# Kernel tuning notes

Measured on AMD Instinct MI355X. Metric: run time of the kernel, lower is better.

Reference implementation:

```python
import jax, jax.numpy as jnp
import numpy as np

ALPHA = 0.2  # LeakyReLU negative slope

def setup_inputs() -> dict:
    key = jax.random.key(0)
    k1, k2, k3, k4 = jax.random.split(key, 4)
    B, N, IN_C, OUT_C = 4, 4096, 64, 64
    features = jax.random.normal(k1, (B, N, IN_C), dtype=jnp.float32)
    adj = jax.random.uniform(k2, (B, N, N), dtype=jnp.float32)  # unused by the module's math
    # xavier_normal approximations
    W = jax.random.normal(k3, (IN_C, OUT_C), dtype=jnp.float32) * np.sqrt(2.0 / (IN_C + OUT_C))
    a = jax.random.normal(k4, (2 * OUT_C, 1), dtype=jnp.float32) * np.sqrt(2.0 / (2 * OUT_C + 1))
    return {"features": features, "adj": adj, "W": W, "a": a}

def reference(features, adj, W, a):
    # h: [B, N, F]
    h = jnp.matmul(features, W)
    out_c = W.shape[1]
    a1 = a[:out_c, 0]   # [F]
    a2 = a[out_c:, 0]   # [F]
    # e[b,i,j] = leakyrelu(h_i . a1 + h_j . a2)  (decomposed; avoids O(N^2*2F) concat)
    s1 = jnp.einsum('bnf,f->bn', h, a1)  # [B, N]
    s2 = jnp.einsum('bnf,f->bn', h, a2)  # [B, N]
    e = s1[:, :, None] + s2[:, None, :]  # [B, N, N]
    e = jnp.where(e >= 0, e, ALPHA * e)  # leaky relu
    attention = jax.nn.softmax(e, axis=2)  # note: adj is NOT used (faithful to source)
    h_prime = jnp.matmul(attention, h)  # [B, N, F]
    return h_prime
```

## Files before the change

kernel.cpp:

```cpp
#include <hip/hip_runtime.h>
#include <hip/hip_bf16.h>
#include <cmath>

#define LRALPHA 0.2f

namespace {
constexpr int BB = 4;
constexpr int NN = 4096;
constexpr int ROWS = BB * NN;
}

typedef __attribute__((ext_vector_type(8))) short bf16x8;
typedef __attribute__((ext_vector_type(4))) float f32x4;

static __device__ inline short f2bf(float x) {
  __hip_bfloat16 t = __float2bfloat16(x);
  return *reinterpret_cast<short*>(&t);
}
static __device__ inline float bf2f(short x) {
  __hip_bfloat16 t = *reinterpret_cast<__hip_bfloat16*>(&x);
  return __bfloat162float(t);
}
static __device__ inline unsigned int packRNE(float a, float b) {
  unsigned int ua = __float_as_uint(a), ub = __float_as_uint(b);
  unsigned int ra = ua + 0x7FFFu + ((ua >> 16) & 1u);
  unsigned int rb = ub + 0x7FFFu + ((ub >> 16) & 1u);
  return (ra >> 16) | (rb & 0xFFFF0000u);
}

__global__ __launch_bounds__(256) void k_hcvt(
    const float* __restrict__ feat, const float* __restrict__ W,
    const float* __restrict__ a,
    unsigned short* __restrict__ hTh, unsigned short* __restrict__ hTl,
    float* __restrict__ Ag, float* __restrict__ Apg,
    float* __restrict__ Bv, float* __restrict__ Bpv) {
  __shared__ float tile[64][65];
  const int lane = threadIdx.x & 63;
  const int wave = threadIdx.x >> 6;
  const int row0 = blockIdx.x * 64;

  float wreg[64];
#pragma unroll
  for (int k = 0; k < 64; ++k) wreg[k] = W[k * 64 + lane];
  const float a1 = a[lane], a2 = a[64 + lane];

  for (int r = 0; r < 16; ++r) {
    const int row = row0 + wave * 16 + r;
    const float4* f4 = (const float4*)(feat + (size_t)row * 64);
    float hv = 0.f;
#pragma unroll
    for (int kk = 0; kk < 16; ++kk) {
      float4 f = f4[kk];
      hv = fmaf(f.x, wreg[4 * kk + 0], hv);
      hv = fmaf(f.y, wreg[4 * kk + 1], hv);
      hv = fmaf(f.z, wreg[4 * kk + 2], hv);
      hv = fmaf(f.w, wreg[4 * kk + 3], hv);
    }
    tile[wave * 16 + r][lane] = hv;
    float p1 = hv * a1, p2 = hv * a2;
#pragma unroll
    for (int off = 32; off; off >>= 1) {
      p1 += __shfl_xor(p1, off, 64);
      p2 += __shfl_xor(p2, off, 64);
    }
    if (lane == 0) {
      Ag[row]  = expf(p1);
      Apg[row] = expf(LRALPHA * p1);
      Bv[row]  = expf(p2);
      Bpv[row] = expf(LRALPHA * p2);
    }
  }
  __syncthreads();

  const int b = row0 >> 12;
  const int n0 = row0 & (NN - 1);
  const size_t base = ((size_t)b << 18) + ((size_t)(n0 >> 3) << 9)
                    + ((size_t)(lane >> 3) << 9) + (lane & 7);
#pragma unroll
  for (int cc = 0; cc < 16; ++cc) {
    int ch = cc * 4 + wave;
    float v = tile[lane][ch];
    short hi = f2bf(v);
    short lo = f2bf(v - bf2f(hi));
    size_t idx = base + (ch << 3);
    hTh[idx] = (unsigned short)hi;
    hTl[idx] = (unsigned short)lo;
  }
}

__global__ __launch_bounds__(512, 4) void k_attn(
    const unsigned short* __restrict__ hTh, const unsigned short* __restrict__ hTl,
    const float* __restrict__ Ag, const float* __restrict__ Apg,
    const float* __restrict__ Bv, const float* __restrict__ Bpv,
    float* __restrict__ out) {
  __shared__ float slab[4][32][65];
  __shared__ float l_lds[4][32];

  const int wave = threadIdx.x >> 6;
  const int lane = threadIdx.x & 63;
  const int m = lane & 15;
  const int quad = lane >> 4;
  const int row0 = blockIdx.x * 32;
  const int b = row0 >> 12;
  const int i0 = row0 + m, i1 = row0 + 16 + m;

  const float Ar0 = Ag[i0], Ap0 = Apg[i0];
  const float Ar1 = Ag[i1], Ap1 = Apg[i1];

  f32x4 acc00 = {0,0,0,0}, acc01 = {0,0,0,0}, acc02 = {0,0,0,0}, acc03 = {0,0,0,0};
  f32x4 acc10 = {0,0,0,0}, acc11 = {0,0,0,0}, acc12 = {0,0,0,0}, acc13 = {0,0,0,0};
  f32x4 lacc0 = {0,0,0,0}, lacc1 = {0,0,0,0};

  bf16x8 ones;
#pragma unroll
  for (int e = 0; e < 8; ++e) ones[e] = (short)0x3F80;

  const int j0 = wave * (NN / 8) + quad * 8;
  const float4* Bq4  = (const float4*)(Bv  + (b << 12) + j0);
  const float4* Bpq4 = (const float4*)(Bpv + (b << 12) + j0);
  const unsigned short* hp = hTh + ((size_t)b << 18)
                           + ((size_t)(j0 >> 3) << 9) + (m << 3);
  const unsigned short* lp = hTl + ((size_t)b << 18)
                           + ((size_t)(j0 >> 3) << 9) + (m << 3);
  constexpr int ITERS = NN / 8 / 32;

  float4 bA = Bq4[0], bB = Bq4[1];
  float4 pA = Bpq4[0], pB = Bpq4[1];

  for (int it = 0; it < ITERS; ++it) {
    Bq4 += 8; Bpq4 += 8;
    float4 nbA = Bq4[0], nbB = Bq4[1];
    float4 npA = Bpq4[0], npB = Bpq4[1];

    bf16x8 hh0 = *(const bf16x8*)(hp);
    bf16x8 hh1 = *(const bf16x8*)(hp + 128);
    bf16x8 hh2 = *(const bf16x8*)(hp + 256);
    bf16x8 hh3 = *(const bf16x8*)(hp + 384);
    bf16x8 hl0 = *(const bf16x8*)(lp);
    bf16x8 hl1 = *(const bf16x8*)(lp + 128);
    bf16x8 hl2 = *(const bf16x8*)(lp + 256);
    bf16x8 hl3 = *(const bf16x8*)(lp + 384);

    float bvv[8] = {bA.x, bA.y, bA.z, bA.w, bB.x, bB.y, bB.z, bB.w};
    float pvv[8] = {pA.x, pA.y, pA.z, pA.w, pB.x, pB.y, pB.z, pB.w};

    float w0v[8], w1v[8];
#pragma unroll
    for (int e = 0; e < 8; ++e) {
      float Bj = bvv[e], Bpj = pvv[e];
      w0v[e] = fmaxf(Ar0 * Bj, Ap0 * Bpj);
      w1v[e] = fmaxf(Ar1 * Bj, Ap1 * Bpj);
    }
    union { bf16x8 v; unsigned int u[4]; } af0u, af1u;
#pragma unroll
    for (int p = 0; p < 4; ++p) {
      af0u.u[p] = packRNE(w0v[2 * p], w0v[2 * p + 1]);
      af1u.u[p] = packRNE(w1v[2 * p], w1v[2 * p + 1]);
    }
    bf16x8 af0 = af0u.v, af1 = af1u.v;

    lacc0 = __builtin_amdgcn_mfma_f32_16x16x32_bf16(af0, ones, lacc0, 0, 0, 0);
    lacc1 = __builtin_amdgcn_mfma_f32_16x16x32_bf16(af1, ones, lacc1, 0, 0, 0);
    acc00 = __builtin_amdgcn_mfma_f32_16x16x32_bf16(af0, hh0, acc00, 0, 0, 0);
    acc00 = __builtin_amdgcn_mfma_f32_16x16x32_bf16(af0, hl0, acc00, 0, 0, 0);
    acc01 = __builtin_amdgcn_mfma_f32_16x16x32_bf16(af0, hh1, acc01, 0, 0, 0);
    acc01 = __builtin_amdgcn_mfma_f32_16x16x32_bf16(af0, hl1, acc01, 0, 0, 0);
    acc02 = __builtin_amdgcn_mfma_f32_16x16x32_bf16(af0, hh2, acc02, 0, 0, 0);
    acc02 = __builtin_amdgcn_mfma_f32_16x16x32_bf16(af0, hl2, acc02, 0, 0, 0);
    acc03 = __builtin_amdgcn_mfma_f32_16x16x32_bf16(af0, hh3, acc03, 0, 0, 0);
    acc03 = __builtin_amdgcn_mfma_f32_16x16x32_bf16(af0, hl3, acc03, 0, 0, 0);
    acc10 = __builtin_amdgcn_mfma_f32_16x16x32_bf16(af1, hh0, acc10, 0, 0, 0);
    acc10 = __builtin_amdgcn_mfma_f32_16x16x32_bf16(af1, hl0, acc10, 0, 0, 0);
    acc11 = __builtin_amdgcn_mfma_f32_16x16x32_bf16(af1, hh1, acc11, 0, 0, 0);
    acc11 = __builtin_amdgcn_mfma_f32_16x16x32_bf16(af1, hl1, acc11, 0, 0, 0);
    acc12 = __builtin_amdgcn_mfma_f32_16x16x32_bf16(af1, hh2, acc12, 0, 0, 0);
    acc12 = __builtin_amdgcn_mfma_f32_16x16x32_bf16(af1, hl2, acc12, 0, 0, 0);
    acc13 = __builtin_amdgcn_mfma_f32_16x16x32_bf16(af1, hh3, acc13, 0, 0, 0);
    acc13 = __builtin_amdgcn_mfma_f32_16x16x32_bf16(af1, hl3, acc13, 0, 0, 0);

    hp += 2048; lp += 2048;
    bA = nbA; bB = nbB; pA = npA; pB = npB;
  }

  const int sidx = wave & 3;
  if (wave < 4) {
#pragma unroll
    for (int reg = 0; reg < 4; ++reg) {
      int rl = quad * 4 + reg;
      slab[sidx][rl][m]      = acc00[reg];
      slab[sidx][rl][m + 16] = acc01[reg];
      slab[sidx][rl][m + 32] = acc02[reg];
      slab[sidx][rl][m + 48] = acc03[reg];
      slab[sidx][16 + rl][m]      = acc10[reg];
      slab[sidx][16 + rl][m + 16] = acc11[reg];
      slab[sidx][16 + rl][m + 32] = acc12[reg];
      slab[sidx][16 + rl][m + 48] = acc13[reg];
    }
    if (m == 0) {
#pragma unroll
      for (int reg = 0; reg < 4; ++reg) {
        l_lds[sidx][quad * 4 + reg]      = lacc0[reg];
        l_lds[sidx][16 + quad * 4 + reg] = lacc1[reg];
      }
    }
  }
  __syncthreads();
  if (wave >= 4) {
#pragma unroll
    for (int reg = 0; reg < 4; ++reg) {
      int rl = quad * 4 + reg;
      slab[sidx][rl][m]      += acc00[reg];
      slab[sidx][rl][m + 16] += acc01[reg];
      slab[sidx][rl][m + 32] += acc02[reg];
      slab[sidx][rl][m + 48] += acc03[reg];
      slab[sidx][16 + rl][m]      += acc10[reg];
      slab[sidx][16 + rl][m + 16] += acc11[reg];
      slab[sidx][16 + rl][m + 32] += acc12[reg];
      slab[sidx][16 + rl][m + 48] += acc13[reg];
    }
    if (m == 0) {
#pragma unroll
      for (int reg = 0; reg < 4; ++reg) {
        l_lds[sidx][quad * 4 + reg]      += lacc0[reg];
        l_lds[sidx][16 + quad * 4 + reg] += lacc1[reg];
      }
    }
  }
  __syncthreads();

#pragma unroll
  for (int k = 0; k < 4; ++k) {
    int f = threadIdx.x + 512 * k;
    int rl = f >> 6, c = f & 63;
    float s = slab[0][rl][c] + slab[1][rl][c] + slab[2][rl][c] + slab[3][rl][c];
    float L = l_lds[0][rl] + l_lds[1][rl] + l_lds[2][rl] + l_lds[3][rl];
    out[((size_t)(row0 + rl)) * 64 + c] = s / L;
  }
}


extern "C" void kernel_launch(void* const* d_in, const int* in_sizes, int n_in,
                              void* d_out, int out_size, void* d_ws, size_t ws_size,
                              hipStream_t stream) {
  const float* feat = (const float*)d_in[0];
  const float* W = (const float*)d_in[2];
  const float* a = (const float*)d_in[3];
  float* out = (float*)d_out;

  char* ws = (char*)d_ws;
  size_t off = 0;
  auto carve = [&](size_t bytes) -> char* {
    char* p = ws + off;
    off = (off + bytes + 255) & ~(size_t)255;
    return p;
  };
  unsigned short* hTh = (unsigned short*)carve((size_t)ROWS * 64 * sizeof(unsigned short));
  unsigned short* hTl = (unsigned short*)carve((size_t)ROWS * 64 * sizeof(unsigned short));
  float* Ag    = (float*)carve(ROWS * sizeof(float));
  float* Apg   = (float*)carve(ROWS * sizeof(float));
  float* Bv    = (float*)carve((ROWS + 64) * sizeof(float));
  float* Bpv   = (float*)carve((ROWS + 64) * sizeof(float));

  k_hcvt<<<ROWS / 64, 256, 0, stream>>>(feat, W, a, hTh, hTl, Ag, Apg, Bv, Bpv);
  k_attn<<<ROWS / 32, 512, 0, stream>>>(hTh, hTl, Ag, Apg, Bv, Bpv, out);
}
```

Baseline: 351.5 us.

## Replace split bf16 hi/lo MFMA with single fp16 MFMA and prefetch h

Stores h as a single fp16 copy instead of a bf16 high/low pair, so each inner iteration issues 10 MFMAs instead of 18 and loads half as much h data. Attention weights are also converted to fp16 directly, with no manual RNE packing. The h loads are software-pipelined one iteration ahead, and the workspace is padded so the final prefetch stays in bounds. fp16 carries fewer mantissa bits than the bf16 hi+lo pair and has a narrow exponent range, so the exp-based weights risk overflow or underflow and the result is less accurate.

Measured after the change: 343.9 us. -2.2%, faster.

```diff
diff --git a/kernel.cpp b/kernel.cpp
--- a/kernel.cpp
+++ b/kernel.cpp
@@ -1,5 +1,4 @@
 #include <hip/hip_runtime.h>
-#include <hip/hip_bf16.h>
 #include <cmath>
 
 #define LRALPHA 0.2f
@@ -10,28 +9,13 @@
 constexpr int ROWS = BB * NN;
 }
 
-typedef __attribute__((ext_vector_type(8))) short bf16x8;
+typedef __attribute__((ext_vector_type(8))) _Float16 f16x8;
 typedef __attribute__((ext_vector_type(4))) float f32x4;
-
-static __device__ inline short f2bf(float x) {
-  __hip_bfloat16 t = __float2bfloat16(x);
-  return *reinterpret_cast<short*>(&t);
-}
-static __device__ inline float bf2f(short x) {
-  __hip_bfloat16 t = *reinterpret_cast<__hip_bfloat16*>(&x);
-  return __bfloat162float(t);
-}
-static __device__ inline unsigned int packRNE(float a, float b) {
-  unsigned int ua = __float_as_uint(a), ub = __float_as_uint(b);
-  unsigned int ra = ua + 0x7FFFu + ((ua >> 16) & 1u);
-  unsigned int rb = ub + 0x7FFFu + ((ub >> 16) & 1u);
-  return (ra >> 16) | (rb & 0xFFFF0000u);
-}
 
 __global__ __launch_bounds__(256) void k_hcvt(
     const float* __restrict__ feat, const float* __restrict__ W,
     const float* __restrict__ a,
-    unsigned short* __restrict__ hTh, unsigned short* __restrict__ hTl,
+    unsigned short* __restrict__ hT,
     float* __restrict__ Ag, float* __restrict__ Apg,
     float* __restrict__ Bv, float* __restrict__ Bpv) {
   __shared__ float tile[64][65];
@@ -80,16 +64,13 @@
   for (int cc = 0; cc < 16; ++cc) {
     int ch = cc * 4 + wave;
     float v = tile[lane][ch];
-    short hi = f2bf(v);
-    short lo = f2bf(v - bf2f(hi));
-    size_t idx = base + (ch << 3);
-    hTh[idx] = (unsigned short)hi;
-    hTl[idx] = (unsigned short)lo;
+    _Float16 hv16 = (_Float16)v;
+    hT[base + (ch << 3)] = *reinterpret_cast<unsigned short*>(&hv16);
   }
 }
 
 __global__ __launch_bounds__(512, 4) void k_attn(
-    const unsigned short* __restrict__ hTh, const unsigned short* __restrict__ hTl,
+    const unsigned short* __restrict__ hT,
     const float* __restrict__ Ag, const float* __restrict__ Apg,
     const float* __restrict__ Bv, const float* __restrict__ Bpv,
     float* __restrict__ out) {
@@ -111,75 +92,58 @@
   f32x4 acc10 = {0,0,0,0}, acc11 = {0,0,0,0}, acc12 = {0,0,0,0}, acc13 = {0,0,0,0};
   f32x4 lacc0 = {0,0,0,0}, lacc1 = {0,0,0,0};
 
-  bf16x8 ones;
-#pragma unroll
-  for (int e = 0; e < 8; ++e) ones[e] = (short)0x3F80;
+  f16x8 ones;
+#pragma unroll
+  for (int e = 0; e < 8; ++e) ones[e] = (_Float16)1.0f;
 
   const int j0 = wave * (NN / 8) + quad * 8;
   const float4* Bq4  = (const float4*)(Bv  + (b << 12) + j0);
   const float4* Bpq4 = (const float4*)(Bpv + (b << 12) + j0);
-  const unsigned short* hp = hTh + ((size_t)b << 18)
-                           + ((size_t)(j0 >> 3) << 9) + (m << 3);
-  const unsigned short* lp = hTl + ((size_t)b << 18)
+  const unsigned short* hp = hT + ((size_t)b << 18)
                            + ((size_t)(j0 >> 3) << 9) + (m << 3);
   constexpr int ITERS = NN / 8 / 32;
 
   float4 bA = Bq4[0], bB = Bq4[1];
   float4 pA = Bpq4[0], pB = Bpq4[1];
+  f16x8 hh0 = *(const f16x8*)(hp);
+  f16x8 hh1 = *(const f16x8*)(hp + 128);
+  f16x8 hh2 = *(const f16x8*)(hp + 256);
+  f16x8 hh3 = *(const f16x8*)(hp + 384);
 
   for (int it = 0; it < ITERS; ++it) {
     Bq4 += 8; Bpq4 += 8;
+    hp += 2048;
     float4 nbA = Bq4[0], nbB = Bq4[1];
     float4 npA = Bpq4[0], npB = Bpq4[1];
-
-    bf16x8 hh0 = *(const bf16x8*)(hp);
-    bf16x8 hh1 = *(const bf16x8*)(hp + 128);
-    bf16x8 hh2 = *(const bf16x8*)(hp + 256);
-    bf16x8 hh3 = *(const bf16x8*)(hp + 384);
-    bf16x8 hl0 = *(const bf16x8*)(lp);
-    bf16x8 hl1 = *(const bf16x8*)(lp + 128);
-    bf16x8 hl2 = *(const bf16x8*)(lp + 256);
-    bf16x8 hl3 = *(const bf16x8*)(lp + 384);
+    f16x8 nh0 = *(const f16x8*)(hp);
+    f16x8 nh1 = *(const f16x8*)(hp + 128);
+    f16x8 nh2 = *(const f16x8*)(hp + 256);
+    f16x8 nh3 = *(const f16x8*)(hp + 384);
 
     float bvv[8] = {bA.x, bA.y, bA.z, bA.w, bB.x, bB.y, bB.z, bB.w};
     float pvv[8] = {pA.x, pA.y, pA.z, pA.w, pB.x, pB.y, pB.z, pB.w};
 
-    float w0v[8], w1v[8];
+    f16x8 af0, af1;
 #pragma unroll
     for (int e = 0; e < 8; ++e) {
       float Bj = bvv[e], Bpj = pvv[e];
-      w0v[e] = fmaxf(Ar0 * Bj, Ap0 * Bpj);
-      w1v[e] = fmaxf(Ar1 * Bj, Ap1 * Bpj);
-    }
-    union { bf16x8 v; unsigned int u[4]; } af0u, af1u;
-#pragma unroll
-    for (int p = 0; p < 4; ++p) {
-      af0u.u[p] = packRNE(w0v[2 * p], w0v[2 * p + 1]);
-      af1u.u[p] = packRNE(w1v[2 * p], w1v[2 * p + 1]);
-    }
-    bf16x8 af0 = af0u.v, af1 = af1u.v;
-
-    lacc0 = __builtin_amdgcn_mfma_f32_16x16x32_bf16(af0, ones, lacc0, 0, 0, 0);
-    lacc1 = __builtin_amdgcn_mfma_f32_16x16x32_bf16(af1, ones, lacc1, 0, 0, 0);
-    acc00 = __builtin_amdgcn_mfma_f32_16x16x32_bf16(af0, hh0, acc00, 0, 0, 0);
-    acc00 = __builtin_amdgcn_mfma_f32_16x16x32_bf16(af0, hl0, acc00, 0, 0, 0);
-    acc01 = __builtin_amdgcn_mfma_f32_16x16x32_bf16(af0, hh1, acc01, 0, 0, 0);
-    acc01 = __builtin_amdgcn_mfma_f32_16x16x32_bf16(af0, hl1, acc01, 0, 0, 0);
-    acc02 = __builtin_amdgcn_mfma_f32_16x16x32_bf16(af0, hh2, acc02, 0, 0, 0);
-    acc02 = __builtin_amdgcn_mfma_f32_16x16x32_bf16(af0, hl2, acc02, 0, 0, 0);
-    acc03 = __builtin_amdgcn_mfma_f32_16x16x32_bf16(af0, hh3, acc03, 0, 0, 0);
-    acc03 = __builtin_amdgcn_mfma_f32_16x16x32_bf16(af0, hl3, acc03, 0, 0, 0);
-    acc10 = __builtin_amdgcn_mfma_f32_16x16x32_bf16(af1, hh0, acc10, 0, 0, 0);
-    acc10 = __builtin_amdgcn_mfma_f32_16x16x32_bf16(af1, hl0, acc10, 0, 0, 0);
-    acc11 = __builtin_amdgcn_mfma_f32_16x16x32_bf16(af1, hh1, acc11, 0, 0, 0);
-    acc11 = __builtin_amdgcn_mfma_f32_16x16x32_bf16(af1, hl1, acc11, 0, 0, 0);
-    acc12 = __builtin_amdgcn_mfma_f32_16x16x32_bf16(af1, hh2, acc12, 0, 0, 0);
-    acc12 = __builtin_amdgcn_mfma_f32_16x16x32_bf16(af1, hl2, acc12, 0, 0, 0);
-    acc13 = __builtin_amdgcn_mfma_f32_16x16x32_bf16(af1, hh3, acc13, 0, 0, 0);
-    acc13 = __builtin_amdgcn_mfma_f32_16x16x32_bf16(af1, hl3, acc13, 0, 0, 0);
-
-    hp += 2048; lp += 2048;
+      af0[e] = (_Float16)fmaxf(Ar0 * Bj, Ap0 * Bpj);
+      af1[e] = (_Float16)fmaxf(Ar1 * Bj, Ap1 * Bpj);
+    }
+
+    lacc0 = __builtin_amdgcn_mfma_f32_16x16x32_f16(af0, ones, lacc0, 0, 0, 0);
+    lacc1 = __builtin_amdgcn_mfma_f32_16x16x32_f16(af1, ones, lacc1, 0, 0, 0);
+    acc00 = __builtin_amdgcn_mfma_f32_16x16x32_f16(af0, hh0, acc00, 0, 0, 0);
+    acc01 = __builtin_amdgcn_mfma_f32_16x16x32_f16(af0, hh1, acc01, 0, 0, 0);
+    acc02 = __builtin_amdgcn_mfma_f32_16x16x32_f16(af0, hh2, acc02, 0, 0, 0);
+    acc03 = __builtin_amdgcn_mfma_f32_16x16x32_f16(af0, hh3, acc03, 0, 0, 0);
+    acc10 = __builtin_amdgcn_mfma_f32_16x16x32_f16(af1, hh0, acc10, 0, 0, 0);
+    acc11 = __builtin_amdgcn_mfma_f32_16x16x32_f16(af1, hh1, acc11, 0, 0, 0);
+    acc12 = __builtin_amdgcn_mfma_f32_16x16x32_f16(af1, hh2, acc12, 0, 0, 0);
+    acc13 = __builtin_amdgcn_mfma_f32_16x16x32_f16(af1, hh3, acc13, 0, 0, 0);
+
     bA = nbA; bB = nbB; pA = npA; pB = npB;
+    hh0 = nh0; hh1 = nh1; hh2 = nh2; hh3 = nh3;
   }
 
   const int sidx = wave & 3;
@@ -254,13 +218,12 @@
     off = (off + bytes + 255) & ~(size_t)255;
     return p;
   };
-  unsigned short* hTh = (unsigned short*)carve((size_t)ROWS * 64 * sizeof(unsigned short));
-  unsigned short* hTl = (unsigned short*)carve((size_t)ROWS * 64 * sizeof(unsigned short));
+  unsigned short* hT = (unsigned short*)carve(((size_t)ROWS * 64 + 4096) * sizeof(unsigned short));
   float* Ag    = (float*)carve(ROWS * sizeof(float));
   float* Apg   = (float*)carve(ROWS * sizeof(float));
   float* Bv    = (float*)carve((ROWS + 64) * sizeof(float));
   float* Bpv   = (float*)carve((ROWS + 64) * sizeof(float));
 
-  k_hcvt<<<ROWS / 64, 256, 0, stream>>>(feat, W, a, hTh, hTl, Ag, Apg, Bv, Bpv);
-  k_attn<<<ROWS / 32, 512, 0, stream>>>(hTh, hTl, Ag, Apg, Bv, Bpv, out);
-}
+  k_hcvt<<<ROWS / 64, 256, 0, stream>>>(feat, W, a, hT, Ag, Apg, Bv, Bpv);
+  k_attn<<<ROWS / 32, 512, 0, stream>>>(hT, Ag, Apg, Bv, Bpv, out);
+}
```
